# Optimization experiments

Measured on AMD Instinct MI355X. Metric: run time of the kernel, lower is better.

## Reference

```python
import jax, jax.numpy as jnp
import numpy as np

INPUT_DIM = 1024
LATENT_DIM = 256
NUM_EMB = 8192
BATCH = 8192


def setup_inputs() -> dict:
    key = jax.random.key(0)
    ks = jax.random.split(key, 6)
    x = jax.random.normal(ks[0], (BATCH, INPUT_DIM), dtype=jnp.float32)
    # torch nn.Linear stores weight as [out, in]
    enc_w = jax.random.normal(ks[1], (LATENT_DIM, INPUT_DIM), dtype=jnp.float32) / np.sqrt(INPUT_DIM)
    enc_b = jnp.zeros((LATENT_DIM,), dtype=jnp.float32)
    # embeddings initialized uniform(-1/K, 1/K) as in the module
    emb = jax.random.uniform(ks[2], (NUM_EMB, LATENT_DIM), dtype=jnp.float32,
                             minval=-1.0 / NUM_EMB, maxval=1.0 / NUM_EMB)
    dec_w = jax.random.normal(ks[3], (INPUT_DIM, LATENT_DIM), dtype=jnp.float32) / np.sqrt(LATENT_DIM)
    dec_b = jnp.zeros((INPUT_DIM,), dtype=jnp.float32)
    return {"x": x, "enc_w": enc_w, "enc_b": enc_b, "emb": emb,
            "dec_w": dec_w, "dec_b": dec_b}


def reference(x, enc_w, enc_b, emb, dec_w, dec_b):
    # encoder: z = x @ W_e^T + b_e  -> [B, D]
    z = x @ enc_w.T + enc_b
    # cosine distance to codebook: d = 1 - <z, e> / (||z|| ||e||)  -> [B, K]
    z_norm = jnp.linalg.norm(z, axis=1, keepdims=True)          # [B, 1]
    e_norm = jnp.linalg.norm(emb, axis=1)                        # [K]
    d = 1.0 - (z @ emb.T) / (z_norm * e_norm)
    idx = jnp.argmin(d, axis=1)                                  # [B]
    # one-hot @ codebook == direct gather of nearest code vectors
    z_q = jnp.take(emb, idx, axis=0)                             # [B, D]
    # straight-through: decoder input z + stop_grad(z_q - z)
    dec_in = z + jax.lax.stop_gradient(z_q - z)
    x_recon = dec_in @ dec_w.T + dec_b
    return (x_recon, z, z_q, idx.astype(jnp.int32))
```

## Files before the change

### kernel.cpp

```cpp
#include <hip/hip_runtime.h>
#include <math.h>

#define BATCH   8192
#define IN_DIM  1024
#define LAT     256
#define NEMB    8192

#define TAU 3.5e-3f

#define RESC_R 16

typedef _Float16 f16x8 __attribute__((ext_vector_type(8)));
typedef _Float16 f16x4 __attribute__((ext_vector_type(4)));
typedef float f32x16_t __attribute__((ext_vector_type(16)));

typedef __attribute__((address_space(1))) const unsigned int gu32_t;
typedef __attribute__((address_space(3))) unsigned int lu32_t;

__device__ __forceinline__ unsigned int ford(float x) {
  unsigned int u = __float_as_uint(x);
  return (u & 0x80000000u) ? ~u : (u | 0x80000000u);
}
__device__ __forceinline__ float funord(unsigned int t) {
  unsigned int u = (t & 0x80000000u) ? (t & 0x7FFFFFFFu) : ~t;
  return __uint_as_float(u);
}

__global__ __launch_bounds__(256) void emb_norms(
    const float* __restrict__ emb, float* __restrict__ inv_norm) {
  int row = blockIdx.x * 4 + (threadIdx.x >> 6);
  int lane = threadIdx.x & 63;
  const float* p = emb + (size_t)row * LAT;
  float s = 0.f;
#pragma unroll
  for (int t = 0; t < 4; ++t) {
    float v = p[lane + 64 * t];
    s += v * v;
  }
#pragma unroll
  for (int off = 32; off; off >>= 1) s += __shfl_xor(s, off);
  if (lane == 0) inv_norm[row] = 1.0f / sqrtf(s);
}

__global__ __launch_bounds__(256) void split16(
    const float* __restrict__ src, const float* __restrict__ inv_norm,
    _Float16* __restrict__ dst, size_t lo_off, int KD, int write_lo) {
  int gw = (blockIdx.x * 256 + threadIdx.x) >> 6;
  int l = threadIdx.x & 63;
  int tile = gw / KD, kb = gw % KD;
  int row = tile * 32 + (l & 31);
  int k = kb * 16 + (l >> 5) * 8;
  const float* p = src + (size_t)row * (KD * 16) + k;
  float scale = inv_norm ? inv_norm[row] : 1.0f;
  f16x8 h, lo;
#pragma unroll
  for (int j = 0; j < 8; ++j) {
    float v = p[j] * scale;
    _Float16 hh = (_Float16)v;
    h[j] = hh;
    lo[j] = (_Float16)(v - (float)hh);
  }
  size_t o = ((size_t)gw * 64 + l) * 8;
  *(f16x8*)(dst + o) = h;
  if (write_lo) *(f16x8*)(dst + lo_off + o) = lo;
}

__global__ __launch_bounds__(256) void gemm16_frag(
    const _Float16* __restrict__ Afrag, size_t a_lo_off,
    const _Float16* __restrict__ Bfrag, size_t b_lo_off,
    const float* __restrict__ bias, float* __restrict__ C, int N, int K) {
  __shared__ char lds[32768];
  const int tid = threadIdx.x;
  const int l = tid & 63;
  const int w = tid >> 6;
  const int mt = w & 1, nt = w >> 1;
  const int rb = blockIdx.y * 64, cb = blockIdx.x * 64;
  const int KD = K >> 4;

  f32x16_t acc = (f32x16_t)0.0f;

  for (int s = 0; s < (K >> 6); ++s) {
#pragma unroll
    for (int i = 0; i < 8; ++i) {
      int c = i * 4 + w;
      int isB = c >> 4;
      int cc = c & 15;
      int t32 = cc >> 3, prec = (cc >> 2) & 1, ks = cc & 3;
      int tile = ((isB ? cb : rb) >> 5) + t32;
      int kb = s * 4 + ks;
      const _Float16* base = isB ? Bfrag : Afrag;
      size_t lo = isB ? b_lo_off : a_lo_off;
      const _Float16* src =
          base + (size_t)prec * lo + ((size_t)(tile * KD + kb) * 64 + l) * 8;
      __builtin_amdgcn_global_load_lds((gu32_t*)src,
                                       (lu32_t*)(lds + (c << 10) + l * 16),
                                       16, 0, 0);
    }
    __syncthreads();
#pragma unroll
    for (int ks = 0; ks < 4; ++ks) {
      f16x8 ah = *(const f16x8*)(lds + ((mt * 8 + ks) << 10) + l * 16);
      f16x8 al = *(const f16x8*)(lds + ((mt * 8 + 4 + ks) << 10) + l * 16);
      f16x8 bh = *(const f16x8*)(lds + 16384 + ((nt * 8 + ks) << 10) + l * 16);
      f16x8 bl = *(const f16x8*)(lds + 16384 + ((nt * 8 + 4 + ks) << 10) + l * 16);
      acc = __builtin_amdgcn_mfma_f32_32x32x16_f16(ah, bh, acc, 0, 0, 0);
      acc = __builtin_amdgcn_mfma_f32_32x32x16_f16(ah, bl, acc, 0, 0, 0);
      acc = __builtin_amdgcn_mfma_f32_32x32x16_f16(al, bh, acc, 0, 0, 0);
    }
    __syncthreads();
  }

  int col = cb + nt * 32 + (l & 31);
  float bv = bias[col];
#pragma unroll
  for (int r = 0; r < 16; ++r) {
    int row = rb + mt * 32 + (r & 3) + 8 * (r >> 2) + 4 * (l >> 5);
    C[(size_t)row * N + col] = acc[r] + bv;
  }
}

__global__ __launch_bounds__(256) void gemm16(
    const float* __restrict__ A, const _Float16* __restrict__ Bfrag,
    size_t b_lo_off, const float* __restrict__ bias, float* __restrict__ C,
    int M, int N, int K) {
  __shared__ char lds[32768];
  const int tid = threadIdx.x;
  const int l = tid & 63;
  const int w = tid >> 6;
  const int mt = w & 1, nt = w >> 1;
  const int rb = blockIdx.y * 64, cb = blockIdx.x * 64;
  const int KD = K >> 4;

  f32x16_t acc = (f32x16_t)0.0f;

  for (int s = 0; s < (K >> 6); ++s) {
#pragma unroll
    for (int i = 0; i < 4; ++i) {
      int c = i * 4 + w;
      int bnt = c >> 3, prec = (c >> 2) & 1, ks = c & 3;
      int tile = (cb >> 5) + bnt, ksg = s * 4 + ks;
      const _Float16* src = Bfrag + (size_t)prec * b_lo_off +
                            ((size_t)(tile * KD + ksg) * 64 + l) * 8;
      __builtin_amdgcn_global_load_lds((gu32_t*)src,
                                       (lu32_t*)(lds + 16384 + (c << 10) + l * 16),
                                       16, 0, 0);
    }
#pragma unroll
    for (int t = 0; t < 4; ++t) {
      int flat = t * 256 + tid;
      int r = flat >> 4, c4 = flat & 15;
      float4 v = *(const float4*)&A[(size_t)(rb + r) * K + s * 64 + 4 * c4];
      int kk = 4 * c4;
      int ks = kk >> 4, j = kk & 7;
      int lane2 = (r & 31) + 32 * ((kk >> 3) & 1);
      int mtt = r >> 5;
      f16x4 hv, lv;
      float vv[4] = {v.x, v.y, v.z, v.w};
#pragma unroll
      for (int e = 0; e < 4; ++e) {
        _Float16 h = (_Float16)vv[e];
        hv[e] = h;
        lv[e] = (_Float16)(vv[e] - (float)h);
      }
      int base = ((mtt * 8 + ks) << 10) + lane2 * 16 + j * 2;
      *(f16x4*)(lds + base) = hv;
      *(f16x4*)(lds + base + 4096) = lv;
    }
    __syncthreads();
#pragma unroll
    for (int ks = 0; ks < 4; ++ks) {
      f16x8 ah = *(const f16x8*)(lds + ((mt * 8 + ks) << 10) + l * 16);
      f16x8 al = *(const f16x8*)(lds + ((mt * 8 + 4 + ks) << 10) + l * 16);
      f16x8 bh = *(const f16x8*)(lds + 16384 + ((nt * 8 + ks) << 10) + l * 16);
      f16x8 bl = *(const f16x8*)(lds + 16384 + ((nt * 8 + 4 + ks) << 10) + l * 16);
      acc = __builtin_amdgcn_mfma_f32_32x32x16_f16(ah, bh, acc, 0, 0, 0);
      acc = __builtin_amdgcn_mfma_f32_32x32x16_f16(ah, bl, acc, 0, 0, 0);
      acc = __builtin_amdgcn_mfma_f32_32x32x16_f16(al, bh, acc, 0, 0, 0);
    }
    __syncthreads();
  }

  int col = cb + nt * 32 + (l & 31);
  float bv = bias[col];
#pragma unroll
  for (int r = 0; r < 16; ++r) {
    int row = rb + mt * 32 + (r & 3) + 8 * (r >> 2) + 4 * (l >> 5);
    C[(size_t)row * N + col] = acc[r] + bv;
  }
}

__global__ __launch_bounds__(256) void score_mfma(
    const _Float16* __restrict__ zfrag, const _Float16* __restrict__ efrag,
    unsigned long long* __restrict__ cand1, unsigned int* __restrict__ cand2) {
  __shared__ char lds[32768];
  const int tid = threadIdx.x;
  const int l = tid & 63;
  const int w = tid >> 6;
  const int l16 = l * 16;
  const int csplit = blockIdx.x;
  const int rowgrp = blockIdx.y;

  f16x8 a[16];
  {
    const _Float16* ab =
        zfrag + (((size_t)(rowgrp * 4 + w) * 16) * 64 + l) * 8;
#pragma unroll
    for (int kf = 0; kf < 16; ++kf)
      a[kf] = *(const f16x8*)(ab + (size_t)kf * 512);
  }

  f32x16_t acc[4];
#pragma unroll
  for (int j = 0; j < 4; ++j) acc[j] = (f32x16_t)0.0f;

  float b1[16], b2[16];
  int i1[16];
#pragma unroll
  for (int r = 0; r < 16; ++r) {
    b1[r] = -INFINITY;
    b2[r] = -INFINITY;
    i1[r] = 0;
  }

  const char* efragb =
      (const char*)efrag + ((size_t)csplit * 512 + (size_t)w) * 1024 + l16;
  char* ldsb = lds + (w << 10) + l16;
  const char* ldsr = lds + l16;

#pragma unroll
  for (int nt = 0; nt < 4; ++nt)
    __builtin_amdgcn_global_load_lds((gu32_t*)(efragb + nt * 16384),
                                     (lu32_t*)(ldsb + (nt << 12)), 16, 0, 0);

  for (int chunk = 0; chunk < 8; ++chunk) {
#pragma unroll
    for (int s = 0; s < 4; ++s) {
      if (s < 3) {
        const char* sb = efragb + (size_t)chunk * 65536 + (s + 1) * 4096;
        char* db = ldsb + ((s + 1) & 1) * 16384;
#pragma unroll
        for (int nt = 0; nt < 4; ++nt)
          __builtin_amdgcn_global_load_lds((gu32_t*)(sb + nt * 16384),
                                           (lu32_t*)(db + (nt << 12)), 16, 0, 0);
        asm volatile("s_waitcnt vmcnt(4)" ::: "memory");
      } else if (chunk < 7) {
        const char* sb = efragb + (size_t)(chunk + 1) * 65536;
        char* db = ldsb;
#pragma unroll
        for (int nt = 0; nt < 4; ++nt)
          __builtin_amdgcn_global_load_lds((gu32_t*)(sb + nt * 16384),
                                           (lu32_t*)(db + (nt << 12)), 16, 0, 0);
        asm volatile("s_waitcnt vmcnt(4)" ::: "memory");
      } else {
        asm volatile("s_waitcnt vmcnt(0)" ::: "memory");
      }
      __builtin_amdgcn_s_barrier();
      __builtin_amdgcn_sched_barrier(0);
#pragma unroll
      for (int ks = 0; ks < 4; ++ks) {
#pragma unroll
        for (int j = 0; j < 4; ++j) {
          f16x8 bh = *(const f16x8*)(ldsr + ((s & 1) * 16384) + (j << 12) +
                                     (ks << 10));
          acc[j] = __builtin_amdgcn_mfma_f32_32x32x16_f16(a[s * 4 + ks], bh,
                                                          acc[j], 0, 0, 0);
        }
      }
      __builtin_amdgcn_sched_barrier(0);
      __builtin_amdgcn_s_barrier();
    }

    const int colbase = csplit * 1024 + chunk * 128 + (l & 31);
#pragma unroll
    for (int r = 0; r < 16; ++r) {
      float c1 = acc[0][r], c2 = -INFINITY;
      int cidx = colbase;
#pragma unroll
      for (int j = 1; j < 4; ++j) {
        float v = acc[j][r];
        if (v > c1) {
          c2 = c1;
          c1 = v;
          cidx = colbase + j * 32;
        } else {
          c2 = fmaxf(c2, v);
        }
      }
      float nb2 = fmaxf(fminf(b1[r], c1), fmaxf(b2[r], c2));
      if (c1 > b1[r] || (c1 == b1[r] && cidx < i1[r])) {
        b1[r] = c1;
        i1[r] = cidx;
      }
      b2[r] = nb2;
    }
#pragma unroll
    for (int j = 0; j < 4; ++j) acc[j] = (f32x16_t)0.0f;
  }

#pragma unroll
  for (int r = 0; r < 16; ++r) {
    float v1 = b1[r], v2 = b2[r];
    int vi = i1[r];
#pragma unroll
    for (int m = 1; m < 32; m <<= 1) {
      float o1 = __shfl_xor(v1, m);
      int oi = __shfl_xor(vi, m);
      float o2 = __shfl_xor(v2, m);
      float n2v = fmaxf(fminf(v1, o1), fmaxf(v2, o2));
      if (o1 > v1 || (o1 == v1 && oi < vi)) {
        v1 = o1;
        vi = oi;
      }
      v2 = n2v;
    }
    if ((l & 31) == 0) {
      int row = rowgrp * 128 + w * 32 + (r & 3) + 8 * (r >> 2) + 4 * (l >> 5);
      cand1[(size_t)row * 8 + csplit] =
          ((unsigned long long)ford(v1) << 32) |
          (unsigned long long)(unsigned int)(NEMB - 1 - vi);
      cand2[(size_t)row * 8 + csplit] = ford(v2);
    }
  }
}

__global__ __launch_bounds__(256) void finalize1(
    const unsigned long long* __restrict__ cand1,
    const unsigned int* __restrict__ cand2, int* __restrict__ idxi,
    unsigned int* __restrict__ flags, unsigned int* __restrict__ flag_count,
    unsigned int* __restrict__ flag_list) {
  int row = blockIdx.x * 256 + threadIdx.x;
  unsigned long long best = 0;
  unsigned int second = 0;
  int bslot = 0;
#pragma unroll
  for (int s = 0; s < 8; ++s) {
    unsigned long long v = cand1[(size_t)row * 8 + s];
    unsigned int vs = (unsigned int)(v >> 32);
    if (v > best) {
      second = (unsigned int)(best >> 32);
      best = v;
      bslot = s;
    } else if (vs > second) {
      second = vs;
    }
  }
  unsigned int r2 = cand2[(size_t)row * 8 + bslot];
  if (r2 > second) second = r2;
  float s1 = funord((unsigned int)(best >> 32));
  float s2 = funord(second);
  int idx = NEMB - 1 - (int)(best & 0xFFFFFFFFull);
  idxi[row] = idx;
  unsigned int fl = ((s1 - s2) < TAU) ? 1u : 0u;
  flags[row] = fl;
  if (fl) {
    unsigned int p = atomicAdd(flag_count, 1u);
    flag_list[p] = row;
  }
}

__global__ __launch_bounds__(256) void rescore(
    const float* __restrict__ z, const float* __restrict__ emb,
    const float* __restrict__ inv_norm,
    const unsigned int* __restrict__ flag_list,
    const unsigned int* __restrict__ flag_count,
    unsigned long long* __restrict__ packed_rescore) {
  __shared__ float z_s[2][292];
  __shared__ unsigned long long red[64];
  const int tid = threadIdx.x;
  const int l = tid & 63;
  const int w = tid >> 6;
  const int cl = l & 7;
  const int p = l >> 3;
  const int code = w * 8 + cl;
  const int cbase = blockIdx.x * 32;
  const unsigned int rc = blockIdx.y;

  unsigned int cnt = *flag_count;
  if (2 * rc >= cnt) return;

  float4 e4[8];
  const float* ebase = emb + (size_t)(cbase + code) * 256 + p * 32;
#pragma unroll
  for (int j = 0; j < 8; ++j) e4[j] = *(const float4*)&ebase[4 * j];
  const float inv = inv_norm[cbase + code];
  const unsigned int lowbits = (unsigned int)(NEMB - 1 - (cbase + code));

  for (unsigned int f = 2 * rc; f < cnt; f += 2 * RESC_R) {
    int row0 = (int)flag_list[f];
    int row1 = (f + 1 < cnt) ? (int)flag_list[f + 1] : row0;
    __syncthreads();
    if (tid < 128) {
      int half = tid >> 6, t = tid & 63;
      int k0 = t * 4;
      int addr = k0 + 4 * (k0 >> 5);
      const float* zp = z + (size_t)(half ? row1 : row0) * 256 + k0;
      *(float4*)&z_s[half][addr] = *(const float4*)zp;
    }
    __syncthreads();
    float a0 = 0.f, a1 = 0.f;
#pragma unroll
    for (int j = 0; j < 8; ++j) {
      float4 z0 = *(const float4*)&z_s[0][p * 36 + 4 * j];
      float4 z1 = *(const float4*)&z_s[1][p * 36 + 4 * j];
      a0 += e4[j].x * z0.x + e4[j].y * z0.y + e4[j].z * z0.z + e4[j].w * z0.w;
      a1 += e4[j].x * z1.x + e4[j].y * z1.y + e4[j].z * z1.z + e4[j].w * z1.w;
    }
#pragma unroll
    for (int m = 8; m < 64; m <<= 1) {
      a0 += __shfl_xor(a0, m);
      a1 += __shfl_xor(a1, m);
    }
    if (l < 8)
      red[w * 8 + cl] = ((unsigned long long)ford(a0 * inv) << 32) | lowbits;
    else if (l < 16)
      red[32 + w * 8 + cl] = ((unsigned long long)ford(a1 * inv) << 32) | lowbits;
    __syncthreads();
    if (w == 0) {
      unsigned long long v = red[l];
#pragma unroll
      for (int m = 1; m < 32; m <<= 1) {
        unsigned long long o = __shfl_xor(v, m);
        if (o > v) v = o;
      }
      if (l == 0) atomicMax(&packed_rescore[row0], v);
      if (l == 32) atomicMax(&packed_rescore[row1], v);
    }
  }
}

__global__ __launch_bounds__(256) void gather_split(
    const int* __restrict__ idxi, const unsigned int* __restrict__ flags,
    const unsigned long long* __restrict__ packed_rescore,
    const float* __restrict__ emb, float* __restrict__ zq,
    float* __restrict__ idx_out, _Float16* __restrict__ zqfrag,
    size_t lo_off, int use_frag) {
  __shared__ float zrow[32][260];
  __shared__ int idxs[32];
  const int tid = threadIdx.x;
  const int tile = blockIdx.x;
  if (tid < 32) {
    int row = tile * 32 + tid;
    int idx = idxi[row];
    if (flags[row]) idx = NEMB - 1 - (int)(packed_rescore[row] & 0xFFFFFFFFull);
    idxs[tid] = idx;
    idx_out[row] = (float)idx;
  }
  __syncthreads();
#pragma unroll
  for (int t = 0; t < 8; ++t) {
    int flat = t * 256 + tid;
    int r = flat >> 6, c4 = flat & 63;
    float4 v = *(const float4*)&emb[(size_t)idxs[r] * 256 + 4 * c4];
    *(float4*)&zrow[r][4 * c4] = v;
    *(float4*)&zq[(size_t)(tile * 32 + r) * 256 + 4 * c4] = v;
  }
  if (use_frag) {
    __syncthreads();
#pragma unroll
    for (int t = 0; t < 4; ++t) {
      int flat = t * 256 + tid;
      int fb = flat >> 6, fl = flat & 63;
      int r = fl & 31, k0 = fb * 16 + (fl >> 5) * 8;
      float4 v0 = *(const float4*)&zrow[r][k0];
      float4 v1 = *(const float4*)&zrow[r][k0 + 4];
      float vv[8] = {v0.x, v0.y, v0.z, v0.w, v1.x, v1.y, v1.z, v1.w};
      f16x8 hv, lv;
#pragma unroll
      for (int j = 0; j < 8; ++j) {
        _Float16 h = (_Float16)vv[j];
        hv[j] = h;
        lv[j] = (_Float16)(vv[j] - (float)h);
      }
      size_t g = ((size_t)(tile * 16 + fb) * 64 + fl) * 8;
      *(f16x8*)(zqfrag + g) = hv;
      *(f16x8*)(zqfrag + lo_off + g) = lv;
    }
  }
}

extern "C" void kernel_launch(void* const* d_in, const int* in_sizes, int n_in,
                              void* d_out, int out_size, void* d_ws,
                              size_t ws_size, hipStream_t stream) {
  (void)in_sizes; (void)n_in; (void)out_size;
  const float* x     = (const float*)d_in[0];
  const float* enc_w = (const float*)d_in[1];
  const float* enc_b = (const float*)d_in[2];
  const float* emb   = (const float*)d_in[3];
  const float* dec_w = (const float*)d_in[4];
  const float* dec_b = (const float*)d_in[5];

  float* out     = (float*)d_out;
  float* x_recon = out;
  float* z_out   = x_recon + (size_t)BATCH * IN_DIM;
  float* zq_out  = z_out + (size_t)BATCH * LAT;
  float* idx_out = zq_out + (size_t)BATCH * LAT;

  char* ws = (char*)d_ws;
  float* inv_norm = (float*)ws;
  unsigned int* flags = (unsigned int*)(ws + 32768);
  int* idxi = (int*)(ws + 65536);
  unsigned int* flag_count = (unsigned int*)(ws + 98304);
  unsigned long long* packed_rescore =
      (unsigned long long*)(ws + 98432);
  unsigned int* flag_list = (unsigned int*)(ws + 163968);
  unsigned long long* cand1 = (unsigned long long*)(ws + 262144);
  unsigned int* cand2 = (unsigned int*)(ws + 786432);
  _Float16* wfrag  = (_Float16*)(ws + 1048576);
  _Float16* dwfrag = (_Float16*)(ws + 2097152);
  _Float16* efrag  = (_Float16*)(ws + 3145728);
  _Float16* zfrag  = (_Float16*)(ws + 7340032);
  _Float16* zqfrag = (_Float16*)(ws + 15728640);
  _Float16* xfrag  = (_Float16*)(ws + 24117248);

  const bool has_zq = ws_size >= 24117248ull;
  const bool has_x  = ws_size >= 57671680ull;

  hipMemsetAsync(ws + 98304, 0, 128 + 65536, stream);

  emb_norms<<<NEMB / 4, 256, 0, stream>>>(emb, inv_norm);
  split16<<<128, 256, 0, stream>>>(enc_w, (const float*)nullptr, wfrag,
                                   (size_t)LAT * IN_DIM, IN_DIM / 16, 1);
  split16<<<128, 256, 0, stream>>>(dec_w, (const float*)nullptr, dwfrag,
                                   (size_t)IN_DIM * LAT, LAT / 16, 1);
  split16<<<1024, 256, 0, stream>>>(emb, inv_norm, efrag, 0, LAT / 16, 0);

  if (has_x) {
    split16<<<4096, 256, 0, stream>>>(x, (const float*)nullptr, xfrag,
                                      (size_t)BATCH * IN_DIM, IN_DIM / 16, 1);
    gemm16_frag<<<dim3(LAT / 64, BATCH / 64), 256, 0, stream>>>(
        xfrag, (size_t)BATCH * IN_DIM, wfrag, (size_t)LAT * IN_DIM, enc_b,
        z_out, LAT, IN_DIM);
  } else {
    gemm16<<<dim3(LAT / 64, BATCH / 64), 256, 0, stream>>>(
        x, wfrag, (size_t)LAT * IN_DIM, enc_b, z_out, BATCH, LAT, IN_DIM);
  }

  split16<<<1024, 256, 0, stream>>>(z_out, (const float*)nullptr, zfrag,
                                    (size_t)BATCH * LAT, LAT / 16, 0);

  score_mfma<<<dim3(8, 64), 256, 0, stream>>>(zfrag, efrag, cand1, cand2);

  finalize1<<<32, 256, 0, stream>>>(cand1, cand2, idxi, flags, flag_count,
                                    flag_list);
  rescore<<<dim3(256, RESC_R), 256, 0, stream>>>(
      z_out, emb, inv_norm, flag_list, flag_count, packed_rescore);

  gather_split<<<BATCH / 32, 256, 0, stream>>>(
      idxi, flags, packed_rescore, emb, zq_out, idx_out,
      has_zq ? zqfrag : (_Float16*)nullptr, (size_t)BATCH * LAT,
      has_zq ? 1 : 0);

  if (has_zq) {
    gemm16_frag<<<dim3(IN_DIM / 64, BATCH / 64), 256, 0, stream>>>(
        zqfrag, (size_t)BATCH * LAT, dwfrag, (size_t)IN_DIM * LAT, dec_b,
        x_recon, IN_DIM, LAT);
  } else {
    gemm16<<<dim3(IN_DIM / 64, BATCH / 64), 256, 0, stream>>>(
        zq_out, dwfrag, (size_t)IN_DIM * LAT, dec_b, x_recon, BATCH, IN_DIM,
        LAT);
  }
}
```

Measured before the change: 274.2 us.

## Split score kernel over 16 codebook slices with triple-buffered LDS pipeline

Doubles the number of codebook column splits in the scoring kernel, from 8 to 16, so each block handles 512 codes and the grid grows to 1024 blocks for more parallelism. The LDS staging changes from double to triple buffering, which lets the trailing barrier after each stage be dropped and cuts synchronisation per step. The candidate buffers move to a larger workspace region, and finalize now reduces 16 candidates per row. The cost is more LDS per block, which may lower occupancy, more reloading of the z fragments, and extra finalize work.

```diff
diff --git a/kernel.cpp b/kernel.cpp
--- a/kernel.cpp
+++ b/kernel.cpp
@@ -9,6 +9,8 @@
 #define TAU 3.5e-3f
 
 #define RESC_R 16
+
+#define CSPLIT 16
 
 typedef _Float16 f16x8 __attribute__((ext_vector_type(8)));
 typedef _Float16 f16x4 __attribute__((ext_vector_type(4)));
@@ -192,7 +194,7 @@
 __global__ __launch_bounds__(256) void score_mfma(
     const _Float16* __restrict__ zfrag, const _Float16* __restrict__ efrag,
     unsigned long long* __restrict__ cand1, unsigned int* __restrict__ cand2) {
-  __shared__ char lds[32768];
+  __shared__ char lds[49152];
   const int tid = threadIdx.x;
   const int l = tid & 63;
   const int w = tid >> 6;
@@ -223,7 +225,7 @@
   }
 
   const char* efragb =
-      (const char*)efrag + ((size_t)csplit * 512 + (size_t)w) * 1024 + l16;
+      (const char*)efrag + (size_t)csplit * 262144 + (size_t)w * 1024 + l16;
   char* ldsb = lds + (w << 10) + l16;
   const char* ldsr = lds + l16;
 
@@ -232,20 +234,15 @@
     __builtin_amdgcn_global_load_lds((gu32_t*)(efragb + nt * 16384),
                                      (lu32_t*)(ldsb + (nt << 12)), 16, 0, 0);
 
-  for (int chunk = 0; chunk < 8; ++chunk) {
+#pragma unroll
+  for (int chunk = 0; chunk < 4; ++chunk) {
 #pragma unroll
     for (int s = 0; s < 4; ++s) {
-      if (s < 3) {
-        const char* sb = efragb + (size_t)chunk * 65536 + (s + 1) * 4096;
-        char* db = ldsb + ((s + 1) & 1) * 16384;
-#pragma unroll
-        for (int nt = 0; nt < 4; ++nt)
-          __builtin_amdgcn_global_load_lds((gu32_t*)(sb + nt * 16384),
-                                           (lu32_t*)(db + (nt << 12)), 16, 0, 0);
-        asm volatile("s_waitcnt vmcnt(4)" ::: "memory");
-      } else if (chunk < 7) {
-        const char* sb = efragb + (size_t)(chunk + 1) * 65536;
-        char* db = ldsb;
+      const int p = chunk * 4 + s;
+      const int pn = p + 1;
+      if (pn < 16) {
+        const char* sb = efragb + (pn >> 2) * 65536 + (pn & 3) * 4096;
+        char* db = ldsb + (pn % 3) * 16384;
 #pragma unroll
         for (int nt = 0; nt < 4; ++nt)
           __builtin_amdgcn_global_load_lds((gu32_t*)(sb + nt * 16384),
@@ -256,21 +253,20 @@
       }
       __builtin_amdgcn_s_barrier();
       __builtin_amdgcn_sched_barrier(0);
+      const int rb = (p % 3) * 16384;
 #pragma unroll
       for (int ks = 0; ks < 4; ++ks) {
 #pragma unroll
         for (int j = 0; j < 4; ++j) {
-          f16x8 bh = *(const f16x8*)(ldsr + ((s & 1) * 16384) + (j << 12) +
-                                     (ks << 10));
+          f16x8 bh = *(const f16x8*)(ldsr + rb + (j << 12) + (ks << 10));
           acc[j] = __builtin_amdgcn_mfma_f32_32x32x16_f16(a[s * 4 + ks], bh,
                                                           acc[j], 0, 0, 0);
         }
       }
       __builtin_amdgcn_sched_barrier(0);
-      __builtin_amdgcn_s_barrier();
-    }
-
-    const int colbase = csplit * 1024 + chunk * 128 + (l & 31);
+    }
+
+    const int colbase = csplit * 512 + chunk * 128 + (l & 31);
 #pragma unroll
     for (int r = 0; r < 16; ++r) {
       float c1 = acc[0][r], c2 = -INFINITY;
@@ -315,10 +311,10 @@
     }
     if ((l & 31) == 0) {
       int row = rowgrp * 128 + w * 32 + (r & 3) + 8 * (r >> 2) + 4 * (l >> 5);
-      cand1[(size_t)row * 8 + csplit] =
+      cand1[(size_t)row * CSPLIT + csplit] =
           ((unsigned long long)ford(v1) << 32) |
           (unsigned long long)(unsigned int)(NEMB - 1 - vi);
-      cand2[(size_t)row * 8 + csplit] = ford(v2);
+      cand2[(size_t)row * CSPLIT + csplit] = ford(v2);
     }
   }
 }
@@ -333,8 +329,8 @@
   unsigned int second = 0;
   int bslot = 0;
 #pragma unroll
-  for (int s = 0; s < 8; ++s) {
-    unsigned long long v = cand1[(size_t)row * 8 + s];
+  for (int s = 0; s < CSPLIT; ++s) {
+    unsigned long long v = cand1[(size_t)row * CSPLIT + s];
     unsigned int vs = (unsigned int)(v >> 32);
     if (v > best) {
       second = (unsigned int)(best >> 32);
@@ -344,7 +340,7 @@
       second = vs;
     }
   }
-  unsigned int r2 = cand2[(size_t)row * 8 + bslot];
+  unsigned int r2 = cand2[(size_t)row * CSPLIT + bslot];
   if (r2 > second) second = r2;
   float s1 = funord((unsigned int)(best >> 32));
   float s2 = funord(second);
@@ -503,12 +499,12 @@
   unsigned long long* packed_rescore =
       (unsigned long long*)(ws + 98432);
   unsigned int* flag_list = (unsigned int*)(ws + 163968);
-  unsigned long long* cand1 = (unsigned long long*)(ws + 262144);
-  unsigned int* cand2 = (unsigned int*)(ws + 786432);
   _Float16* wfrag  = (_Float16*)(ws + 1048576);
   _Float16* dwfrag = (_Float16*)(ws + 2097152);
   _Float16* efrag  = (_Float16*)(ws + 3145728);
   _Float16* zfrag  = (_Float16*)(ws + 7340032);
+  unsigned long long* cand1 = (unsigned long long*)(ws + 11534336);
+  unsigned int* cand2 = (unsigned int*)(ws + 12582912);
   _Float16* zqfrag = (_Float16*)(ws + 15728640);
   _Float16* xfrag  = (_Float16*)(ws + 24117248);
 
@@ -538,7 +534,7 @@
   split16<<<1024, 256, 0, stream>>>(z_out, (const float*)nullptr, zfrag,
                                     (size_t)BATCH * LAT, LAT / 16, 0);
 
-  score_mfma<<<dim3(8, 64), 256, 0, stream>>>(zfrag, efrag, cand1, cand2);
+  score_mfma<<<dim3(CSPLIT, 64), 256, 0, stream>>>(zfrag, efrag, cand1, cand2);
 
   finalize1<<<32, 256, 0, stream>>>(cand1, cand2, idxi, flags, flag_count,
                                     flag_list);
```

Result: slower. 380.1 us (+38.6%).
